# Performance work log

Hardware: AMD Instinct MI355X
Metric: run time of the kernel (lower is better)

The kernel has to match this reference:

```python
import jax, jax.numpy as jnp
import numpy as np
from jax import lax

# Poincare ball, curvature c = 1.0 (geoopt default for CustomPoincare)
SQRT_C = 1.0
BALL_EPS = 1e-3   # projx margin (geoopt-style)
MIN_NORM = 1e-7
BN_EPS = 1e-5


def _norm(x):
    # norm over channel (last) dim, clamped away from 0
    return jnp.maximum(jnp.linalg.norm(x, axis=-1, keepdims=True), MIN_NORM)


def projx(x):
    # clip points back inside the ball of radius (1-eps)/sqrt(c)
    maxnorm = (1.0 - BALL_EPS) / SQRT_C
    n = _norm(x)
    return x * jnp.minimum(1.0, maxnorm / n)


def expmap0(v):
    # exp map at the origin: tanh(sqrt(c)||v||) * v / (sqrt(c)||v||)
    n = _norm(v)
    return projx(jnp.tanh(SQRT_C * n) * v / (SQRT_C * n))


def logmap0(x):
    # log map at the origin: artanh(sqrt(c)||x||) * x / (sqrt(c)||x||)
    n = _norm(x)
    t = jnp.minimum(SQRT_C * n, 1.0 - 1e-5)
    return jnp.arctanh(t) * x / (SQRT_C * n)


def setup_inputs() -> dict:
    key = jax.random.key(0)
    k0, k1 = jax.random.split(key)
    B, C_in, H, W, C_out = 16, 3, 224, 224, 64
    x = jax.random.normal(k0, (B, C_in, H, W), dtype=jnp.float32)
    # Kaiming-ish init for the 3x3 stem conv, HWIO layout
    fan_in = 3 * 3 * C_in
    conv_w = jax.random.normal(k1, (3, 3, C_in, C_out), dtype=jnp.float32) * np.float32(np.sqrt(2.0 / fan_in))
    conv_b = jnp.zeros((C_out,), dtype=jnp.float32)
    bn_gamma = jnp.ones((C_out,), dtype=jnp.float32)
    bn_beta = jnp.zeros((C_out,), dtype=jnp.float32)
    return {"x": x, "conv_w": conv_w, "conv_b": conv_b,
            "bn_gamma": bn_gamma, "bn_beta": bn_beta}


def reference(x, conv_w, conv_b, bn_gamma, bn_beta):
    # x: [B, C, H, W] -> NHWC (channel-last points on the Poincare ball)
    h = jnp.transpose(x, (0, 2, 3, 1))
    h = projx(h)

    # --- PoincareConv2d: tangent-space 3x3 conv (log0 -> conv+bias -> exp0) ---
    u = logmap0(h)
    u = lax.conv_general_dilated(
        u, conv_w, window_strides=(1, 1), padding="SAME",
        dimension_numbers=("NHWC", "HWIO", "NHWC"))
    u = u + conv_b
    h = expmap0(u)

    # --- PoincareBatchNorm2d: tangent-space BN over (B,H,W) per channel ---
    u = logmap0(h)
    mean = jnp.mean(u, axis=(0, 1, 2), keepdims=True)
    var = jnp.var(u, axis=(0, 1, 2), keepdims=True)
    u = (u - mean) * lax.rsqrt(var + BN_EPS) * bn_gamma + bn_beta
    h = expmap0(u)

    # --- PoincareTangentReLU ---
    h = expmap0(jax.nn.relu(logmap0(h)))
    return h  # [B, H, W, C_out]
```

## Files before the change

### kernel.cpp

```cpp
#include <hip/hip_runtime.h>
#include <math.h>

#define B_ 16
#define H_ 224
#define W_ 224
#define HP_ 226
#define WP_ 226
#define CIN_ 3
#define COUT_ 64
#define NPIX_ (B_ * H_ * W_)
#define NPAD_ (B_ * HP_ * WP_)
#define NBLK_ (NPIX_ / 256)
#define MAXNORM_ 0.999f
#define MINN_ 1e-7f
#define TCL_ (1.0f - 1e-5f)
#define LCLAMP_ 3.8002012f
#define BN_EPS_ 1e-5f
#define NF_ ((float)NPIX_)
#define PADW2_ 36

typedef float v4f __attribute__((ext_vector_type(4)));

struct Acc8 { v4f v0, v1, v2, v3, v4, v5, v6, v7; };
#define EACH8(X) X(0) X(1) X(2) X(3) X(4) X(5) X(6) X(7)

__global__ void k0_transform(const float* __restrict__ x, float4* __restrict__ u0p) {
  int idx = blockIdx.x * 256 + threadIdx.x;
  if (idx >= NPAD_) return;
  int b = idx / (HP_ * WP_);
  int r = idx % (HP_ * WP_);
  int yp = r / WP_, xp = r % WP_;
  float4 o = make_float4(0.f, 0.f, 0.f, 0.f);
  if (yp >= 1 && yp <= H_ && xp >= 1 && xp <= W_) {
    const float* xb = x + (size_t)b * (CIN_ * H_ * W_) + (size_t)(yp - 1) * W_ + (xp - 1);
    float v0 = xb[0];
    float v1 = xb[H_ * W_];
    float v2 = xb[2 * H_ * W_];
    float n = sqrtf(fmaf(v0, v0, fmaf(v1, v1, v2 * v2)));
    float ncl = fmaxf(n, MINN_);
    float s = fminf(1.0f, MAXNORM_ / ncl);
    float p0 = v0 * s, p1 = v1 * s, p2 = v2 * s;
    float np_ = fmaxf(sqrtf(fmaf(p0, p0, fmaf(p1, p1, p2 * p2))), MINN_);
    float t = fminf(np_, TCL_);
    float ath = 0.5f * __logf(__fdividef(1.0f + t, 1.0f - t));
    float f = __fdividef(ath, np_);
    o.x = p0 * f; o.y = p1 * f; o.z = p2 * f;
  }
  u0p[idx] = o;
}

#define LOADTAPS()                                                           \
  int bb = pix / (H_ * W_);                                                  \
  int rr = pix % (H_ * W_);                                                  \
  int yy = rr / W_, xx = rr % W_;                                            \
  const float4* base = u0p + ((size_t)bb * HP_ + yy) * WP_ + xx;             \
  float4 T0 = base[0],        T1 = base[1],            T2 = base[2];         \
  float4 T3 = base[WP_],      T4 = base[WP_ + 1],      T5 = base[WP_ + 2];   \
  float4 T6 = base[2 * WP_],  T7 = base[2 * WP_ + 1],  T8 = base[2 * WP_ + 2]; \
  __builtin_amdgcn_sched_barrier(0);

#define INIT8(i) a.v##i = b4[h8 + i];
#define FMA_X(i) a.v##i += in.x * wp[h8 + i];
#define FMA_Y(i) a.v##i += in.y * wp[16 + h8 + i];
#define FMA_Z(i) a.v##i += in.z * wp[32 + h8 + i];
#define TAPF(t, T) { float4 in = T;                                          \
                     const v4f* wp = (const v4f*)(wgt + (t) * 3 * COUT_);    \
                     EACH8(FMA_X) EACH8(FMA_Y) EACH8(FMA_Z) }
#define CONV_HALF(h8v)                                                       \
  { const int h8 = (h8v); const v4f* b4 = (const v4f*)bias;                  \
    EACH8(INIT8)                                                             \
    TAPF(0, T0) TAPF(1, T1) TAPF(2, T2)                                      \
    TAPF(3, T3) TAPF(4, T4) TAPF(5, T5)                                      \
    TAPF(6, T6) TAPF(7, T7) TAPF(8, T8) }

__device__ __forceinline__ v4f vshfl_xor(v4f v, int m) {
  v4f r;
  r.x = __shfl_xor(v.x, m, 64);
  r.y = __shfl_xor(v.y, m, 64);
  r.z = __shfl_xor(v.z, m, 64);
  r.w = __shfl_xor(v.w, m, 64);
  return r;
}
__device__ __forceinline__ v4f vrelu(v4f v) {
  v.x = fmaxf(v.x, 0.f); v.y = fmaxf(v.y, 0.f);
  v.z = fmaxf(v.z, 0.f); v.w = fmaxf(v.w, 0.f);
  return v;
}
__device__ __forceinline__ float hsum(v4f v) { return (v.x + v.y) + (v.z + v.w); }

#define STAGE8() do {                                                        \
  *(v4f*)(row + 0)  = a.v0; *(v4f*)(row + 4)  = a.v1;                        \
  *(v4f*)(row + 8)  = a.v2; *(v4f*)(row + 12) = a.v3;                        \
  *(v4f*)(row + 16) = a.v4; *(v4f*)(row + 20) = a.v5;                        \
  *(v4f*)(row + 24) = a.v6; *(v4f*)(row + 28) = a.v7;                        \
} while (0)

__global__ void __launch_bounds__(256, 4)
k1_stats(const float4* __restrict__ u0p, const float* __restrict__ wgt,
         const float* __restrict__ bias, float* __restrict__ partials) {
  int pix = blockIdx.x * 256 + threadIdx.x;
  __shared__ __align__(16) float stg[4 * 64 * PADW2_];
  __shared__ float scl[256];
  __shared__ float red_s[256], red_q[256];
  int lane = threadIdx.x & 63, wid = threadIdx.x >> 6;
  float* row = stg + (size_t)(wid * 64 + lane) * PADW2_;
  int pr8 = lane >> 3, qi = lane & 7;
  const float* rb = stg + (size_t)wid * 64 * PADW2_ + pr8 * PADW2_ + qi * 4;
  const float* scrow = scl + wid * 64;

  LOADTAPS()
  Acc8 a;
  CONV_HALF(0)
  v4f s2v = (v4f)0.0f;
#define SQ(i) s2v += a.v##i * a.v##i;
  EACH8(SQ)
#undef SQ
  float s2A = hsum(s2v);
  STAGE8();
  __builtin_amdgcn_wave_barrier();

  CONV_HALF(8)
  s2v = (v4f)0.0f;
#define SQ(i) s2v += a.v##i * a.v##i;
  EACH8(SQ)
#undef SQ
  float n2 = s2A + hsum(s2v);
  float n = sqrtf(n2);
  float sc = (n > LCLAMP_) ? __fdividef(LCLAMP_, n) : 1.0f;
  scl[wid * 64 + lane] = sc;
  __builtin_amdgcn_wave_barrier();

  v4f sA = (v4f)0.0f, qA = (v4f)0.0f;
#pragma unroll
  for (int j = 0; j < 8; j++) {
    float g = scrow[j * 8 + pr8];
    v4f v = *(const v4f*)(rb + j * 8 * PADW2_) * g;
    sA += v; qA += v * v;
  }
  sA += vshfl_xor(sA, 8);  qA += vshfl_xor(qA, 8);
  sA += vshfl_xor(sA, 16); qA += vshfl_xor(qA, 16);
  sA += vshfl_xor(sA, 32); qA += vshfl_xor(qA, 32);
  if (lane < 8) {
    *(v4f*)&red_s[wid * 32 + qi * 4] = sA;
    *(v4f*)&red_q[wid * 32 + qi * 4] = qA;
  }
  __builtin_amdgcn_wave_barrier();

  STAGE8();
  __builtin_amdgcn_wave_barrier();
  v4f sB = (v4f)0.0f, qB = (v4f)0.0f;
#pragma unroll
  for (int j = 0; j < 8; j++) {
    float g = scrow[j * 8 + pr8];
    v4f v = *(const v4f*)(rb + j * 8 * PADW2_) * g;
    sB += v; qB += v * v;
  }
  sB += vshfl_xor(sB, 8);  qB += vshfl_xor(qB, 8);
  sB += vshfl_xor(sB, 16); qB += vshfl_xor(qB, 16);
  sB += vshfl_xor(sB, 32); qB += vshfl_xor(qB, 32);
  if (lane < 8) {
    *(v4f*)&red_s[128 + wid * 32 + qi * 4] = sB;
    *(v4f*)&red_q[128 + wid * 32 + qi * 4] = qB;
  }
  __syncthreads();
  int tid = threadIdx.x;
  if (tid < 128) {
    int c = tid & 63;
    int base2 = (c >> 5) * 128 + (c & 31);
    const float* rr2 = (tid < 64) ? red_s : red_q;
    float tot = rr2[base2] + rr2[base2 + 32] + rr2[base2 + 64] + rr2[base2 + 96];
    partials[(size_t)blockIdx.x * 128 + tid] = tot;
  }
}

__global__ void k2_finalize(const float* __restrict__ partials, const float* __restrict__ gamma,
                            float* __restrict__ stats) {
  int c = blockIdx.x;
  int t = threadIdx.x;
  float s = 0.f, q = 0.f;
  for (int i = t; i < NBLK_; i += 256) {
    s += partials[(size_t)i * 128 + c];
    q += partials[(size_t)i * 128 + 64 + c];
  }
  __shared__ float ls[256], lq[256];
  ls[t] = s; lq[t] = q;
  __syncthreads();
#pragma unroll
  for (int off = 128; off > 0; off >>= 1) {
    if (t < off) { ls[t] += ls[t + off]; lq[t] += lq[t + off]; }
    __syncthreads();
  }
  if (t == 0) {
    float mean = ls[0] / NF_;
    float msq  = lq[0] / NF_;
    float var = msq - mean * mean;
    stats[c] = mean;
    stats[64 + c] = gamma[c] / sqrtf(var + BN_EPS_);
  }
}

__global__ void __launch_bounds__(256, 4)
k3_final(const float4* __restrict__ u0p, const float* __restrict__ wgt,
         const float* __restrict__ bias, const float* __restrict__ stats,
         const float* __restrict__ beta, float* __restrict__ out) {
  int pix = blockIdx.x * 256 + threadIdx.x;
  __shared__ __align__(16) float stg[4 * 64 * PADW2_];
  __shared__ float gl[256];
  int lane = threadIdx.x & 63, wid = threadIdx.x >> 6;
  float* row = stg + (size_t)(wid * 64 + lane) * PADW2_;
  int pr8 = lane >> 3, qi = lane & 7;
  const float* rb = stg + (size_t)wid * 64 * PADW2_ + pr8 * PADW2_ + qi * 4;
  const float* grow = gl + wid * 64;
  v4f* outw = (v4f*)out + ((size_t)blockIdx.x * 256 + wid * 64) * 16;

  const v4f* mean4 = (const v4f*)stats;
  const v4f* rg4   = (const v4f*)(stats + 64);
  const v4f* beta4 = (const v4f*)beta;

  LOADTAPS()
  Acc8 a;
  CONV_HALF(0)
  v4f s2v = (v4f)0.0f, r2v = (v4f)0.0f;
#define BNA(i) { a.v##i = (a.v##i - mean4[i]) * rg4[i] + beta4[i];           \
                 s2v += a.v##i * a.v##i; v4f t_ = vrelu(a.v##i); r2v += t_ * t_; }
  EACH8(BNA)
#undef BNA
  float nv2 = hsum(s2v), r2 = hsum(r2v);
  STAGE8();
  __builtin_amdgcn_wave_barrier();

  CONV_HALF(8)
  s2v = (v4f)0.0f; r2v = (v4f)0.0f;
#define BNB(i) { a.v##i = (a.v##i - mean4[8 + i]) * rg4[8 + i] + beta4[8 + i]; \
                 s2v += a.v##i * a.v##i; v4f t_ = vrelu(a.v##i); r2v += t_ * t_; }
  EACH8(BNB)
#undef BNB
  nv2 += hsum(s2v); r2 += hsum(r2v);
  float nv = sqrtf(nv2);
  float sv = (nv > LCLAMP_) ? __fdividef(LCLAMP_, nv) : 1.0f;
  float nw = fmaxf(sv * sqrtf(r2), MINN_);
  float e2 = __expf(2.0f * nw);
  float th = 1.0f - __fdividef(2.0f, e2 + 1.0f);
  float se = __fdividef(th, nw);
  float clip = fminf(1.0f, MAXNORM_ / fmaxf(th, MINN_));
  float g = se * clip * sv;
  gl[wid * 64 + lane] = g;
  __builtin_amdgcn_wave_barrier();

#pragma unroll
  for (int j = 0; j < 8; j++) {
    float gv = grow[j * 8 + pr8];
    v4f v = vrelu(*(const v4f*)(rb + j * 8 * PADW2_)) * gv;
    __builtin_nontemporal_store(v, outw + (j * 8 + pr8) * 16 + qi);
  }
  __builtin_amdgcn_wave_barrier();

  STAGE8();
  __builtin_amdgcn_wave_barrier();
#pragma unroll
  for (int j = 0; j < 8; j++) {
    float gv = grow[j * 8 + pr8];
    v4f v = vrelu(*(const v4f*)(rb + j * 8 * PADW2_)) * gv;
    __builtin_nontemporal_store(v, outw + (j * 8 + pr8) * 16 + 8 + qi);
  }
}

extern "C" void kernel_launch(void* const* d_in, const int* in_sizes, int n_in,
                              void* d_out, int out_size, void* d_ws, size_t ws_size,
                              hipStream_t stream) {
  const float* x     = (const float*)d_in[0];
  const float* wgt   = (const float*)d_in[1];
  const float* bias  = (const float*)d_in[2];
  const float* gamma = (const float*)d_in[3];
  const float* beta  = (const float*)d_in[4];
  float* out = (float*)d_out;

  char* ws = (char*)d_ws;
  float4* u0p      = (float4*)ws;
  float*  partials = (float*)(ws + (size_t)NPAD_ * 16);
  float*  stats    = (float*)(ws + (size_t)NPAD_ * 16 + (size_t)NBLK_ * 128 * 4);

  hipLaunchKernelGGL(k0_transform, dim3((NPAD_ + 255) / 256), dim3(256), 0, stream, x, u0p);
  hipLaunchKernelGGL(k1_stats,     dim3(NBLK_),               dim3(256), 0, stream, u0p, wgt, bias, partials);
  hipLaunchKernelGGL(k2_finalize,  dim3(64),                  dim3(256), 0, stream, partials, gamma, stats);
  hipLaunchKernelGGL(k3_final,     dim3(NBLK_),               dim3(256), 0, stream, u0p, wgt, bias, stats, beta, out);
}
```

Baseline: 306.6 us.

## Compute two adjacent pixels per thread to reuse weights and overlapping taps

```diff
diff --git a/kernel.cpp b/kernel.cpp
--- a/kernel.cpp
+++ b/kernel.cpp
@@ -10,7 +10,7 @@
 #define COUT_ 64
 #define NPIX_ (B_ * H_ * W_)
 #define NPAD_ (B_ * HP_ * WP_)
-#define NBLK_ (NPIX_ / 256)
+#define NBLK2_ (NPIX_ / 512)
 #define MAXNORM_ 0.999f
 #define MINN_ 1e-7f
 #define TCL_ (1.0f - 1e-5f)
@@ -49,29 +49,33 @@
   u0p[idx] = o;
 }
 
-#define LOADTAPS()                                                           \
-  int bb = pix / (H_ * W_);                                                  \
-  int rr = pix % (H_ * W_);                                                  \
+#define LOADTAPS2()                                                          \
+  int bb = px0 / (H_ * W_);                                                  \
+  int rr = px0 % (H_ * W_);                                                  \
   int yy = rr / W_, xx = rr % W_;                                            \
   const float4* base = u0p + ((size_t)bb * HP_ + yy) * WP_ + xx;             \
-  float4 T0 = base[0],        T1 = base[1],            T2 = base[2];         \
-  float4 T3 = base[WP_],      T4 = base[WP_ + 1],      T5 = base[WP_ + 2];   \
-  float4 T6 = base[2 * WP_],  T7 = base[2 * WP_ + 1],  T8 = base[2 * WP_ + 2]; \
+  float4 T00 = base[0],          T01 = base[1];                              \
+  float4 T02 = base[2],          T03 = base[3];                              \
+  float4 T10 = base[WP_],        T11 = base[WP_ + 1];                        \
+  float4 T12 = base[WP_ + 2],    T13 = base[WP_ + 3];                        \
+  float4 T20 = base[2 * WP_],    T21 = base[2 * WP_ + 1];                    \
+  float4 T22 = base[2 * WP_ + 2], T23 = base[2 * WP_ + 3];                   \
   __builtin_amdgcn_sched_barrier(0);
 
-#define INIT8(i) a.v##i = b4[h8 + i];
-#define FMA_X(i) a.v##i += in.x * wp[h8 + i];
-#define FMA_Y(i) a.v##i += in.y * wp[16 + h8 + i];
-#define FMA_Z(i) a.v##i += in.z * wp[32 + h8 + i];
-#define TAPF(t, T) { float4 in = T;                                          \
-                     const v4f* wp = (const v4f*)(wgt + (t) * 3 * COUT_);    \
-                     EACH8(FMA_X) EACH8(FMA_Y) EACH8(FMA_Z) }
-#define CONV_HALF(h8v)                                                       \
-  { const int h8 = (h8v); const v4f* b4 = (const v4f*)bias;                  \
-    EACH8(INIT8)                                                             \
-    TAPF(0, T0) TAPF(1, T1) TAPF(2, T2)                                      \
-    TAPF(3, T3) TAPF(4, T4) TAPF(5, T5)                                      \
-    TAPF(6, T6) TAPF(7, T7) TAPF(8, T8) }
+#define INIT2(i) { v4f bv = b4[h8 + i]; A0_.v##i = bv; A1_.v##i = bv; }
+#define FMA2_X(i) { v4f w = wp[h8 + i];      A0_.v##i += in0.x * w; A1_.v##i += in1.x * w; }
+#define FMA2_Y(i) { v4f w = wp[16 + h8 + i]; A0_.v##i += in0.y * w; A1_.v##i += in1.y * w; }
+#define FMA2_Z(i) { v4f w = wp[32 + h8 + i]; A0_.v##i += in0.z * w; A1_.v##i += in1.z * w; }
+#define TAP2(t, Ta, Tb) { float4 in0 = Ta, in1 = Tb;                         \
+                          const v4f* wp = (const v4f*)(wgt + (t) * 3 * COUT_); \
+                          EACH8(FMA2_X) EACH8(FMA2_Y) EACH8(FMA2_Z) }
+#define CONV2_HALF(h8v, P, Q) {                                              \
+  const int h8 = (h8v); const v4f* b4 = (const v4f*)bias;                    \
+  Acc8& A0_ = P; Acc8& A1_ = Q;                                              \
+  EACH8(INIT2)                                                               \
+  TAP2(0, T00, T01) TAP2(1, T01, T02) TAP2(2, T02, T03)                      \
+  TAP2(3, T10, T11) TAP2(4, T11, T12) TAP2(5, T12, T13)                      \
+  TAP2(6, T20, T21) TAP2(7, T21, T22) TAP2(8, T22, T23) }
 
 __device__ __forceinline__ v4f vshfl_xor(v4f v, int m) {
   v4f r;
@@ -88,82 +92,84 @@
 }
 __device__ __forceinline__ float hsum(v4f v) { return (v.x + v.y) + (v.z + v.w); }
 
-#define STAGE8() do {                                                        \
+#define STAGE8(a) do {                                                       \
   *(v4f*)(row + 0)  = a.v0; *(v4f*)(row + 4)  = a.v1;                        \
   *(v4f*)(row + 8)  = a.v2; *(v4f*)(row + 12) = a.v3;                        \
   *(v4f*)(row + 16) = a.v4; *(v4f*)(row + 20) = a.v5;                        \
   *(v4f*)(row + 24) = a.v6; *(v4f*)(row + 28) = a.v7;                        \
 } while (0)
 
-__global__ void __launch_bounds__(256, 4)
+__global__ void __launch_bounds__(256, 2)
 k1_stats(const float4* __restrict__ u0p, const float* __restrict__ wgt,
          const float* __restrict__ bias, float* __restrict__ partials) {
-  int pix = blockIdx.x * 256 + threadIdx.x;
   __shared__ __align__(16) float stg[4 * 64 * PADW2_];
-  __shared__ float scl[256];
+  __shared__ float scl[512];
   __shared__ float red_s[256], red_q[256];
-  int lane = threadIdx.x & 63, wid = threadIdx.x >> 6;
+  int tid = threadIdx.x, lane = tid & 63, wid = tid >> 6;
+  int px0 = blockIdx.x * 512 + wid * 128 + 2 * lane;
   float* row = stg + (size_t)(wid * 64 + lane) * PADW2_;
   int pr8 = lane >> 3, qi = lane & 7;
   const float* rb = stg + (size_t)wid * 64 * PADW2_ + pr8 * PADW2_ + qi * 4;
-  const float* scrow = scl + wid * 64;
-
-  LOADTAPS()
-  Acc8 a;
-  CONV_HALF(0)
-  v4f s2v = (v4f)0.0f;
-#define SQ(i) s2v += a.v##i * a.v##i;
-  EACH8(SQ)
-#undef SQ
-  float s2A = hsum(s2v);
-  STAGE8();
-  __builtin_amdgcn_wave_barrier();
-
-  CONV_HALF(8)
-  s2v = (v4f)0.0f;
-#define SQ(i) s2v += a.v##i * a.v##i;
-  EACH8(SQ)
-#undef SQ
-  float n2 = s2A + hsum(s2v);
-  float n = sqrtf(n2);
-  float sc = (n > LCLAMP_) ? __fdividef(LCLAMP_, n) : 1.0f;
-  scl[wid * 64 + lane] = sc;
-  __builtin_amdgcn_wave_barrier();
-
-  v4f sA = (v4f)0.0f, qA = (v4f)0.0f;
-#pragma unroll
-  for (int j = 0; j < 8; j++) {
-    float g = scrow[j * 8 + pr8];
-    v4f v = *(const v4f*)(rb + j * 8 * PADW2_) * g;
-    sA += v; qA += v * v;
-  }
+  const float* scw = scl + wid * 128;
+
+  LOADTAPS2()
+  Acc8 a0, a1;
+  CONV2_HALF(0, a0, a1)
+  v4f s2v0 = (v4f)0.0f, s2v1 = (v4f)0.0f;
+#define SQ2(i) { s2v0 += a0.v##i * a0.v##i; s2v1 += a1.v##i * a1.v##i; }
+  EACH8(SQ2)
+#undef SQ2
+  float s2A0 = hsum(s2v0), s2A1 = hsum(s2v1);
+  STAGE8(a0);
+  __builtin_amdgcn_wave_barrier();
+
+  Acc8 c0, c1;
+  CONV2_HALF(8, c0, c1)
+  s2v0 = (v4f)0.0f; s2v1 = (v4f)0.0f;
+#define SQ2(i) { s2v0 += c0.v##i * c0.v##i; s2v1 += c1.v##i * c1.v##i; }
+  EACH8(SQ2)
+#undef SQ2
+  float n0 = sqrtf(s2A0 + hsum(s2v0));
+  float n1 = sqrtf(s2A1 + hsum(s2v1));
+  scl[wid * 128 + 2 * lane]     = (n0 > LCLAMP_) ? __fdividef(LCLAMP_, n0) : 1.0f;
+  scl[wid * 128 + 2 * lane + 1] = (n1 > LCLAMP_) ? __fdividef(LCLAMP_, n1) : 1.0f;
+  __builtin_amdgcn_wave_barrier();
+
+  v4f sA = (v4f)0.0f, qA = (v4f)0.0f, sB = (v4f)0.0f, qB = (v4f)0.0f;
+#define RDROUND(sv, qv, par)                                                 \
+  _Pragma("unroll") for (int j = 0; j < 8; j++) {                            \
+    float g = scw[2 * (j * 8 + pr8) + (par)];                                \
+    v4f v = *(const v4f*)(rb + j * 8 * PADW2_) * g;                          \
+    sv += v; qv += v * v;                                                    \
+  }
+  RDROUND(sA, qA, 0)
+  __builtin_amdgcn_wave_barrier();
+  STAGE8(a1);
+  __builtin_amdgcn_wave_barrier();
+  RDROUND(sA, qA, 1)
+  __builtin_amdgcn_wave_barrier();
+  STAGE8(c0);
+  __builtin_amdgcn_wave_barrier();
+  RDROUND(sB, qB, 0)
+  __builtin_amdgcn_wave_barrier();
+  STAGE8(c1);
+  __builtin_amdgcn_wave_barrier();
+  RDROUND(sB, qB, 1)
+#undef RDROUND
+
   sA += vshfl_xor(sA, 8);  qA += vshfl_xor(qA, 8);
   sA += vshfl_xor(sA, 16); qA += vshfl_xor(qA, 16);
   sA += vshfl_xor(sA, 32); qA += vshfl_xor(qA, 32);
-  if (lane < 8) {
-    *(v4f*)&red_s[wid * 32 + qi * 4] = sA;
-    *(v4f*)&red_q[wid * 32 + qi * 4] = qA;
-  }
-  __builtin_amdgcn_wave_barrier();
-
-  STAGE8();
-  __builtin_amdgcn_wave_barrier();
-  v4f sB = (v4f)0.0f, qB = (v4f)0.0f;
-#pragma unroll
-  for (int j = 0; j < 8; j++) {
-    float g = scrow[j * 8 + pr8];
-    v4f v = *(const v4f*)(rb + j * 8 * PADW2_) * g;
-    sB += v; qB += v * v;
-  }
   sB += vshfl_xor(sB, 8);  qB += vshfl_xor(qB, 8);
   sB += vshfl_xor(sB, 16); qB += vshfl_xor(qB, 16);
   sB += vshfl_xor(sB, 32); qB += vshfl_xor(qB, 32);
   if (lane < 8) {
+    *(v4f*)&red_s[wid * 32 + qi * 4] = sA;
+    *(v4f*)&red_q[wid * 32 + qi * 4] = qA;
     *(v4f*)&red_s[128 + wid * 32 + qi * 4] = sB;
     *(v4f*)&red_q[128 + wid * 32 + qi * 4] = qB;
   }
   __syncthreads();
-  int tid = threadIdx.x;
   if (tid < 128) {
     int c = tid & 63;
     int base2 = (c >> 5) * 128 + (c & 31);
@@ -178,7 +184,7 @@
   int c = blockIdx.x;
   int t = threadIdx.x;
   float s = 0.f, q = 0.f;
-  for (int i = t; i < NBLK_; i += 256) {
+  for (int i = t; i < NBLK2_; i += 256) {
     s += partials[(size_t)i * 128 + c];
     q += partials[(size_t)i * 128 + 64 + c];
   }
@@ -199,70 +205,90 @@
   }
 }
 
-__global__ void __launch_bounds__(256, 4)
+__global__ void __launch_bounds__(256, 2)
 k3_final(const float4* __restrict__ u0p, const float* __restrict__ wgt,
          const float* __restrict__ bias, const float* __restrict__ stats,
          const float* __restrict__ beta, float* __restrict__ out) {
-  int pix = blockIdx.x * 256 + threadIdx.x;
   __shared__ __align__(16) float stg[4 * 64 * PADW2_];
-  __shared__ float gl[256];
-  int lane = threadIdx.x & 63, wid = threadIdx.x >> 6;
+  __shared__ float gl[512];
+  int tid = threadIdx.x, lane = tid & 63, wid = tid >> 6;
+  int px0 = blockIdx.x * 512 + wid * 128 + 2 * lane;
   float* row = stg + (size_t)(wid * 64 + lane) * PADW2_;
   int pr8 = lane >> 3, qi = lane & 7;
   const float* rb = stg + (size_t)wid * 64 * PADW2_ + pr8 * PADW2_ + qi * 4;
-  const float* grow = gl + wid * 64;
-  v4f* outw = (v4f*)out + ((size_t)blockIdx.x * 256 + wid * 64) * 16;
+  const float* glw = gl + wid * 128;
+  v4f* ow = (v4f*)out + ((size_t)blockIdx.x * 512 + wid * 128) * 16;
 
   const v4f* mean4 = (const v4f*)stats;
   const v4f* rg4   = (const v4f*)(stats + 64);
   const v4f* beta4 = (const v4f*)beta;
 
-  LOADTAPS()
-  Acc8 a;
-  CONV_HALF(0)
-  v4f s2v = (v4f)0.0f, r2v = (v4f)0.0f;
-#define BNA(i) { a.v##i = (a.v##i - mean4[i]) * rg4[i] + beta4[i];           \
-                 s2v += a.v##i * a.v##i; v4f t_ = vrelu(a.v##i); r2v += t_ * t_; }
-  EACH8(BNA)
-#undef BNA
-  float nv2 = hsum(s2v), r2 = hsum(r2v);
-  STAGE8();
-  __builtin_amdgcn_wave_barrier();
-
-  CONV_HALF(8)
-  s2v = (v4f)0.0f; r2v = (v4f)0.0f;
-#define BNB(i) { a.v##i = (a.v##i - mean4[8 + i]) * rg4[8 + i] + beta4[8 + i]; \
-                 s2v += a.v##i * a.v##i; v4f t_ = vrelu(a.v##i); r2v += t_ * t_; }
-  EACH8(BNB)
-#undef BNB
-  nv2 += hsum(s2v); r2 += hsum(r2v);
-  float nv = sqrtf(nv2);
-  float sv = (nv > LCLAMP_) ? __fdividef(LCLAMP_, nv) : 1.0f;
-  float nw = fmaxf(sv * sqrtf(r2), MINN_);
-  float e2 = __expf(2.0f * nw);
-  float th = 1.0f - __fdividef(2.0f, e2 + 1.0f);
-  float se = __fdividef(th, nw);
-  float clip = fminf(1.0f, MAXNORM_ / fmaxf(th, MINN_));
-  float g = se * clip * sv;
-  gl[wid * 64 + lane] = g;
-  __builtin_amdgcn_wave_barrier();
-
-#pragma unroll
-  for (int j = 0; j < 8; j++) {
-    float gv = grow[j * 8 + pr8];
-    v4f v = vrelu(*(const v4f*)(rb + j * 8 * PADW2_)) * gv;
-    __builtin_nontemporal_store(v, outw + (j * 8 + pr8) * 16 + qi);
-  }
-  __builtin_amdgcn_wave_barrier();
-
-  STAGE8();
-  __builtin_amdgcn_wave_barrier();
-#pragma unroll
-  for (int j = 0; j < 8; j++) {
-    float gv = grow[j * 8 + pr8];
-    v4f v = vrelu(*(const v4f*)(rb + j * 8 * PADW2_)) * gv;
-    __builtin_nontemporal_store(v, outw + (j * 8 + pr8) * 16 + 8 + qi);
-  }
+  LOADTAPS2()
+  Acc8 a0, a1;
+  CONV2_HALF(0, a0, a1)
+  v4f s0v = (v4f)0.0f, r0v = (v4f)0.0f, s1v = (v4f)0.0f, r1v = (v4f)0.0f;
+#define BN2A(i) {                                                            \
+    a0.v##i = (a0.v##i - mean4[i]) * rg4[i] + beta4[i];                      \
+    s0v += a0.v##i * a0.v##i; v4f t_ = vrelu(a0.v##i); r0v += t_ * t_;       \
+    a1.v##i = (a1.v##i - mean4[i]) * rg4[i] + beta4[i];                      \
+    s1v += a1.v##i * a1.v##i; v4f u_ = vrelu(a1.v##i); r1v += u_ * u_; }
+  EACH8(BN2A)
+#undef BN2A
+  float nv2_0 = hsum(s0v), r2_0 = hsum(r0v);
+  float nv2_1 = hsum(s1v), r2_1 = hsum(r1v);
+  STAGE8(a0);
+  __builtin_amdgcn_wave_barrier();
+
+  Acc8 c0, c1;
+  CONV2_HALF(8, c0, c1)
+  s0v = (v4f)0.0f; r0v = (v4f)0.0f; s1v = (v4f)0.0f; r1v = (v4f)0.0f;
+#define BN2B(i) {                                                            \
+    c0.v##i = (c0.v##i - mean4[8 + i]) * rg4[8 + i] + beta4[8 + i];          \
+    s0v += c0.v##i * c0.v##i; v4f t_ = vrelu(c0.v##i); r0v += t_ * t_;       \
+    c1.v##i = (c1.v##i - mean4[8 + i]) * rg4[8 + i] + beta4[8 + i];          \
+    s1v += c1.v##i * c1.v##i; v4f u_ = vrelu(c1.v##i); r1v += u_ * u_; }
+  EACH8(BN2B)
+#undef BN2B
+  nv2_0 += hsum(s0v); r2_0 += hsum(r0v);
+  nv2_1 += hsum(s1v); r2_1 += hsum(r1v);
+#define OUTSCALE(nv2, r2, dst) {                                             \
+    float nv = sqrtf(nv2);                                                   \
+    float sv = (nv > LCLAMP_) ? __fdividef(LCLAMP_, nv) : 1.0f;              \
+    float nw = fmaxf(sv * sqrtf(r2), MINN_);                                 \
+    float e2 = __expf(2.0f * nw);                                            \
+    float th = 1.0f - __fdividef(2.0f, e2 + 1.0f);                           \
+    float se = __fdividef(th, nw);                                           \
+    float clip = fminf(1.0f, MAXNORM_ / fmaxf(th, MINN_));                   \
+    dst = se * clip * sv; }
+  float g0, g1;
+  OUTSCALE(nv2_0, r2_0, g0)
+  OUTSCALE(nv2_1, r2_1, g1)
+#undef OUTSCALE
+  gl[wid * 128 + 2 * lane]     = g0;
+  gl[wid * 128 + 2 * lane + 1] = g1;
+  __builtin_amdgcn_wave_barrier();
+
+#define STROUND(par, choff)                                                  \
+  _Pragma("unroll") for (int j = 0; j < 8; j++) {                            \
+    int p = 2 * (j * 8 + pr8) + (par);                                       \
+    float g = glw[p];                                                        \
+    v4f v = vrelu(*(const v4f*)(rb + j * 8 * PADW2_)) * g;                   \
+    __builtin_nontemporal_store(v, ow + (size_t)p * 16 + (choff) + qi);      \
+  }
+  STROUND(0, 0)
+  __builtin_amdgcn_wave_barrier();
+  STAGE8(a1);
+  __builtin_amdgcn_wave_barrier();
+  STROUND(1, 0)
+  __builtin_amdgcn_wave_barrier();
+  STAGE8(c0);
+  __builtin_amdgcn_wave_barrier();
+  STROUND(0, 8)
+  __builtin_amdgcn_wave_barrier();
+  STAGE8(c1);
+  __builtin_amdgcn_wave_barrier();
+  STROUND(1, 8)
+#undef STROUND
 }
 
 extern "C" void kernel_launch(void* const* d_in, const int* in_sizes, int n_in,
@@ -278,10 +304,10 @@
   char* ws = (char*)d_ws;
   float4* u0p      = (float4*)ws;
   float*  partials = (float*)(ws + (size_t)NPAD_ * 16);
-  float*  stats    = (float*)(ws + (size_t)NPAD_ * 16 + (size_t)NBLK_ * 128 * 4);
+  float*  stats    = (float*)(ws + (size_t)NPAD_ * 16 + (size_t)NBLK2_ * 128 * 4);
 
   hipLaunchKernelGGL(k0_transform, dim3((NPAD_ + 255) / 256), dim3(256), 0, stream, x, u0p);
-  hipLaunchKernelGGL(k1_stats,     dim3(NBLK_),               dim3(256), 0, stream, u0p, wgt, bias, partials);
+  hipLaunchKernelGGL(k1_stats,     dim3(NBLK2_),              dim3(256), 0, stream, u0p, wgt, bias, partials);
   hipLaunchKernelGGL(k2_finalize,  dim3(64),                  dim3(256), 0, stream, partials, gamma, stats);
-  hipLaunchKernelGGL(k3_final,     dim3(NBLK_),               dim3(256), 0, stream, u0p, wgt, bias, stats, beta, out);
-}
+  hipLaunchKernelGGL(k3_final,     dim3(NBLK2_),              dim3(256), 0, stream, u0p, wgt, bias, stats, beta, out);
+}
```

Result: no change. 312.4 us (+1.9%).
